# Performance work log

Measured on AMD Instinct MI355X. Metric: run time of the kernel, lower is better.

Reference implementation:

```python
import jax, jax.numpy as jnp
import numpy as np

N_NODES = 100000
N_EDGES = 1_600_000


def setup_inputs() -> dict:
    key = jax.random.key(0)
    ks = jax.random.split(key, 18)
    glorot = lambda k, fi, fo: jax.random.normal(k, (fi, fo), jnp.float32) * np.sqrt(2.0 / (fi + fo))
    inp = {
        "x": jax.random.normal(ks[0], (N_NODES, 5), jnp.float32),
        "edge_index": jax.random.randint(ks[1], (2, N_EDGES), 0, N_NODES, jnp.int64 if jax.config.jax_enable_x64 else jnp.int32),
        "W1": glorot(ks[2], 5, 32),  "b1": jnp.zeros((32,), jnp.float32),
        "W2": glorot(ks[3], 32, 32), "b2": jnp.zeros((32,), jnp.float32),
        "W3": glorot(ks[4], 32, 32), "b3": jnp.zeros((32,), jnp.float32),
        "Wd": glorot(ks[5], 32, 1),  "bd": jnp.zeros((1,), jnp.float32),
        "Wa": glorot(ks[6], 32, 1),  "ba": jnp.zeros((1,), jnp.float32),
        "Wt": glorot(ks[7], 32, 2),  "bt": jnp.zeros((2,), jnp.float32),
        "Wact": glorot(ks[8], 32, 9), "bact": jnp.zeros((9,), jnp.float32),
    }
    return inp


def _gcn_layer(x, row, col, norm, W, b):
    # GCNConv(add_self_loops=False): out[col] += norm * (x @ W)[row], then + bias
    h = x @ W                                  # [N, F_out]
    msg = h[row] * norm[:, None]               # [E, F_out]
    return jax.ops.segment_sum(msg, col, num_segments=N_NODES) + b


def reference(x, edge_index, W1, b1, W2, b2, W3, b3, Wd, bd, Wa, ba, Wt, bt, Wact, bact):
    row, col = edge_index[0], edge_index[1]
    # symmetric gcn normalization: deg over targets (unit edge weights)
    deg = jax.ops.segment_sum(jnp.ones((row.shape[0],), x.dtype), col, num_segments=N_NODES)
    dis = jnp.where(deg > 0, jax.lax.rsqrt(jnp.maximum(deg, 1.0)), 0.0)
    norm = dis[row] * dis[col]                 # [E]

    h = jax.nn.relu(_gcn_layer(x, row, col, norm, W1, b1))   # dropout = identity (eval)
    h = jax.nn.relu(_gcn_layer(h, row, col, norm, W2, b2))
    h = jax.nn.relu(_gcn_layer(h, row, col, norm, W3, b3))

    distance_scores = (h @ Wd + bd)[:, 0]      # [N]
    attention_scores = (h @ Wa + ba)[:, 0]     # [N]
    target_idx = jnp.argmax(attention_scores)
    h_t = h[target_idx]                        # [32]
    target_location_score = h_t @ Wt + bt      # [2]
    action_logits = h_t @ Wact + bact          # [9]
    return distance_scores, attention_scores, target_location_score, action_logits
```

## Files before the change

### kernel.cpp

```cpp
#include <hip/hip_runtime.h>
#include <hip/hip_fp16.h>
#include <math.h>


#define N_NODES 100000
#define F 32
#define BUCKET 64
#define NB ((N_NODES + BUCKET - 1) / BUCKET)
#define NBLK 256
#define SMAX 1536
#define TBKT 32
#define NGRP 8
#define RPG (NBLK / NGRP)

__global__ void hist_kernel(const int* __restrict__ col, int* __restrict__ counts, int E,
                            int* __restrict__ ticket) {
    __shared__ int hist[NB];
    int tid = threadIdx.x, blk = blockIdx.x;
    if (blk == 0 && tid == 0) *ticket = 0;
    for (int i = tid; i < NB; i += 1024) hist[i] = 0;
    __syncthreads();
    int chunk = (((E + NBLK - 1) / NBLK) + 1) & ~1;
    int beg = blk * chunk;
    int end = beg + chunk; if (end > E) end = E;
    int cnt = end - beg; if (cnt < 0) cnt = 0;
    int pairs = cnt >> 1;
    const int2* c2 = (const int2*)(col + beg);
    for (int p = tid; p < pairs; p += 1024) {
        int2 v = c2[p];
        atomicAdd(&hist[v.x >> 6], 1);
        atomicAdd(&hist[v.y >> 6], 1);
    }
    if ((cnt & 1) && tid == 0) atomicAdd(&hist[col[end - 1] >> 6], 1);
    __syncthreads();
    for (int i = tid; i < NB; i += 1024) counts[(size_t)blk * NB + i] = hist[i];
}

__global__ void scan_kernel(int* __restrict__ counts, int* __restrict__ tot,
                            int* __restrict__ bucket_base, int* __restrict__ rowstart,
                            int* __restrict__ ticket) {
    __shared__ int tile[NBLK][TBKT];
    __shared__ int wtot[NGRP][TBKT];
    int tid = threadIdx.x;
    int g = tid >> 5, bl = tid & 31;
    int b = blockIdx.x * TBKT + bl;
    bool valid = (b < NB);
    int jbase = g * RPG;
    int run = 0;
#pragma unroll
    for (int r = 0; r < RPG; r++) {
        int j = jbase + r;
        int v = valid ? counts[(size_t)j * NB + b] : 0;
        tile[j][bl] = run;
        run += v;
    }
    wtot[g][bl] = run;
    __syncthreads();
    int off = 0;
#pragma unroll
    for (int gg = 0; gg < NGRP; gg++) {
        int w = wtot[gg][bl];
        if (gg < g) off += w;
    }
    if (valid) {
#pragma unroll
        for (int r = 0; r < RPG; r++) {
            int j = jbase + r;
            counts[(size_t)j * NB + b] = tile[j][bl] + off;
        }
        if (g == NGRP - 1) tot[b] = off + run;
    }
    __shared__ int lastflag;
    __threadfence();
    __syncthreads();
    if (tid == 0) lastflag = (atomicAdd(ticket, 1) == (int)gridDim.x - 1);
    __syncthreads();
    if (!lastflag) return;
    __threadfence();
    constexpr int PER = (NB + 255) / 256;
    __shared__ int bsum[256];
    int base = tid * PER;
    int loc[PER];
    int s = 0;
#pragma unroll
    for (int k = 0; k < PER; k++) {
        int idx = base + k;
        int v = (idx < NB) ? tot[idx] : 0;
        loc[k] = s;
        s += v;
    }
    bsum[tid] = s;
    __syncthreads();
    for (int off2 = 1; off2 < 256; off2 <<= 1) {
        int v = (tid >= off2) ? bsum[tid - off2] : 0;
        __syncthreads();
        bsum[tid] += v;
        __syncthreads();
    }
    int excl = bsum[tid] - s;
#pragma unroll
    for (int k = 0; k < PER; k++) {
        int idx = base + k;
        if (idx < NB) bucket_base[idx] = excl + loc[k];
    }
    if (tid == 255) {
        bucket_base[NB] = bsum[255];
        rowstart[N_NODES] = bsum[255];
    }
}

__global__ void scatter_kernel(const int* __restrict__ row, const int* __restrict__ col,
                               const int* __restrict__ counts, const int* __restrict__ bucket_base,
                               unsigned* __restrict__ storage, int E) {
    __shared__ int cur[NB];
    int tid = threadIdx.x, blk = blockIdx.x;
    for (int i = tid; i < NB; i += 1024)
        cur[i] = counts[(size_t)blk * NB + i] + bucket_base[i];
    __syncthreads();
    int chunk = (((E + NBLK - 1) / NBLK) + 1) & ~1;
    int beg = blk * chunk;
    int end = beg + chunk; if (end > E) end = E;
    int cnt = end - beg; if (cnt < 0) cnt = 0;
    int pairs = cnt >> 1;
    const int2* c2 = (const int2*)(col + beg);
    const int2* r2 = (const int2*)(row + beg);
    for (int p = tid; p < pairs; p += 1024) {
        int2 c = c2[p];
        int2 r = r2[p];
        int pos0 = atomicAdd(&cur[c.x >> 6], 1);
        storage[pos0] = ((unsigned)(c.x & 63) << 17) | (unsigned)r.x;
        int pos1 = atomicAdd(&cur[c.y >> 6], 1);
        storage[pos1] = ((unsigned)(c.y & 63) << 17) | (unsigned)r.y;
    }
    if ((cnt & 1) && tid == 0) {
        int c = col[end - 1], r = row[end - 1];
        int pos = atomicAdd(&cur[c >> 6], 1);
        storage[pos] = ((unsigned)(c & 63) << 17) | (unsigned)r;
    }
}

__global__ void csr_build_kernel(const unsigned* __restrict__ storage, const int* __restrict__ bucket_base,
                                 int* __restrict__ rowstart, int* __restrict__ csr_src,
                                 float* __restrict__ dis, const float* __restrict__ x,
                                 float* __restrict__ xd, int n) {
    __shared__ unsigned sh[SMAX];
    __shared__ int outloc[SMAX];
    __shared__ int hist[BUCKET];
    __shared__ int pre[BUCKET];
    __shared__ int cur[BUCKET];
    __shared__ float dloc[BUCKET];
    int b = blockIdx.x, tid = threadIdx.x;
    if (tid < BUCKET) hist[tid] = 0;
    __syncthreads();
    int base = bucket_base[b];
    int tot = bucket_base[b + 1] - base;
    if (tot > SMAX) tot = SMAX;
    for (int i = tid; i < tot; i += 256) sh[i] = storage[base + i];
    __syncthreads();
    for (int i = tid; i < tot; i += 256) atomicAdd(&hist[sh[i] >> 17], 1);
    __syncthreads();
    if (tid < BUCKET) pre[tid] = hist[tid];
    __syncthreads();
    for (int off = 1; off < BUCKET; off <<= 1) {
        int v = 0;
        if (tid < BUCKET && tid >= off) v = pre[tid - off];
        __syncthreads();
        if (tid < BUCKET && tid >= off) pre[tid] += v;
        __syncthreads();
    }
    if (tid < BUCKET) {
        int excl = pre[tid] - hist[tid];
        cur[tid] = excl;
        int node = b * BUCKET + tid;
        if (node < n) {
            rowstart[node] = base + excl;
            int d = hist[tid];
            float dv = (d > 0) ? rsqrtf((float)d) : 0.0f;
            dis[node] = dv;
            dloc[tid] = dv;
        }
    }
    __syncthreads();
    for (int i = tid; i < BUCKET * 8; i += 256) {
        int nl = i >> 3, f = i & 7;
        int node = b * BUCKET + nl;
        if (node < n) xd[(size_t)node * 8 + f] = (f < 5) ? dloc[nl] * x[(size_t)node * 5 + f] : 0.0f;
    }
    for (int i = tid; i < tot; i += 256) {
        unsigned p = sh[i];
        int pos = atomicAdd(&cur[p >> 17], 1);
        outloc[pos] = (int)(p & 0x1FFFF);
    }
    __syncthreads();
    for (int i = tid; i < tot; i += 256) csr_src[base + i] = outloc[i];
}

__global__ void layer1_fused(const float* __restrict__ xd, const int* __restrict__ rowstart,
                             const int* __restrict__ csr_src, const float* __restrict__ dis,
                             const float* __restrict__ W1, const float* __restrict__ b1,
                             __half* __restrict__ gda, int n) {
    __shared__ float Ws[5 * F];
    __shared__ float s1s[32][8];
    int tid = threadIdx.x;
    if (tid < 5 * F) Ws[tid] = W1[tid];
    int grp = tid >> 3, f = tid & 7;
    int node = blockIdx.x * 32 + grp;
    float sum = 0.0f;
    if (node < n) {
        int start = rowstart[node], end = rowstart[node + 1];
        float a0 = 0, a1 = 0, a2 = 0, a3 = 0, a4 = 0, a5 = 0, a6 = 0, a7 = 0;
        int i = start;
        for (; i + 7 < end; i += 8) {
            int r0 = csr_src[i], r1 = csr_src[i+1], r2 = csr_src[i+2], r3 = csr_src[i+3];
            int r4 = csr_src[i+4], r5 = csr_src[i+5], r6 = csr_src[i+6], r7 = csr_src[i+7];
            a0 += xd[r0*8+f]; a1 += xd[r1*8+f]; a2 += xd[r2*8+f]; a3 += xd[r3*8+f];
            a4 += xd[r4*8+f]; a5 += xd[r5*8+f]; a6 += xd[r6*8+f]; a7 += xd[r7*8+f];
        }
        for (; i < end; i++) a0 += xd[csr_src[i]*8+f];
        sum = ((a0+a1)+(a2+a3)) + ((a4+a5)+(a6+a7));
    }
    s1s[grp][f] = sum;
    __syncthreads();
    if (node < n) {
        float dv = dis[node];
        float sk0 = dv * s1s[grp][0], sk1 = dv * s1s[grp][1], sk2 = dv * s1s[grp][2];
        float sk3 = dv * s1s[grp][3], sk4 = dv * s1s[grp][4];
        int fb = f * 4;
#pragma unroll
        for (int j = 0; j < 4; j++) {
            int ff = fb + j;
            float acc = b1[ff] + sk0 * Ws[0*F+ff] + sk1 * Ws[1*F+ff] + sk2 * Ws[2*F+ff]
                       + sk3 * Ws[3*F+ff] + sk4 * Ws[4*F+ff];
            float h = acc > 0.0f ? acc : 0.0f;
            gda[(size_t)node * F + ff] = __float2half(dv * h);
        }
    }
}

__device__ __forceinline__ void gather8lane(const uint2* __restrict__ gin2,
                                            const int* __restrict__ csr_src,
                                            int start, int end, int l, int E,
                                            float& a0, float& a1, float& a2, float& a3) {
    a0 = a1 = a2 = a3 = 0.0f;
    int i = start;
    if (i + 8 <= end) {
        int safe = i + l; if (safe > E - 1) safe = E - 1;
        int myidx = csr_src[safe];
        while (i + 8 <= end) {
            int nexti = i + 8;
            int nextidx = 0;
            if (nexti + 8 <= end) {
                int s2 = nexti + l; if (s2 > E - 1) s2 = E - 1;
                nextidx = csr_src[s2];
            }
#pragma unroll
            for (int j = 0; j < 8; j++) {
                int r = __shfl(myidx, j, 8);
                uint2 v = gin2[(size_t)r * 8 + l];
                __half2 h0 = *(__half2*)&v.x;
                __half2 h1 = *(__half2*)&v.y;
                float2 f0 = __half22float2(h0);
                float2 f1 = __half22float2(h1);
                a0 += f0.x; a1 += f0.y; a2 += f1.x; a3 += f1.y;
            }
            myidx = nextidx;
            i = nexti;
        }
    }
    for (; i < end; i++) {
        int r = csr_src[i];
        uint2 v = gin2[(size_t)r * 8 + l];
        __half2 h0 = *(__half2*)&v.x;
        __half2 h1 = *(__half2*)&v.y;
        float2 f0 = __half22float2(h0);
        float2 f1 = __half22float2(h1);
        a0 += f0.x; a1 += f0.y; a2 += f1.x; a3 += f1.y;
    }
}

__global__ void layer_mid_fused(const uint2* __restrict__ gin2, const int* __restrict__ rowstart,
                                const int* __restrict__ csr_src, const float* __restrict__ dis,
                                const float* __restrict__ W, const float* __restrict__ bb,
                                uint2* __restrict__ gout2, int n, int E) {
    __shared__ float Ws[F * F];
    __shared__ float hs[32][F + 1];
    int tid = threadIdx.x;
    for (int i = tid; i < F * F; i += 256) Ws[i] = W[i];
    int grp = tid >> 3;
    int l = tid & 7;
    int node = blockIdx.x * 32 + grp;
    int start = rowstart[node], end = rowstart[node + 1];
    float a0, a1, a2, a3;
    gather8lane(gin2, csr_src, start, end, l, E, a0, a1, a2, a3);
    float dv = dis[node];
    int fb = 4 * l;
    hs[grp][fb]     = dv * a0;
    hs[grp][fb + 1] = dv * a1;
    hs[grp][fb + 2] = dv * a2;
    hs[grp][fb + 3] = dv * a3;
    __syncthreads();
    float acc0 = bb[fb], acc1 = bb[fb+1], acc2 = bb[fb+2], acc3 = bb[fb+3];
#pragma unroll
    for (int k = 0; k < F; k++) {
        float hv = hs[grp][k];
        acc0 += hv * Ws[k*F+fb];
        acc1 += hv * Ws[k*F+fb+1];
        acc2 += hv * Ws[k*F+fb+2];
        acc3 += hv * Ws[k*F+fb+3];
    }
    float h0 = acc0 > 0.0f ? acc0 : 0.0f;
    float h1 = acc1 > 0.0f ? acc1 : 0.0f;
    float h2 = acc2 > 0.0f ? acc2 : 0.0f;
    float h3 = acc3 > 0.0f ? acc3 : 0.0f;
    __half2 o0 = __floats2half2_rn(dv * h0, dv * h1);
    __half2 o1 = __floats2half2_rn(dv * h2, dv * h3);
    uint2 pack;
    pack.x = *(unsigned*)&o0;
    pack.y = *(unsigned*)&o1;
    gout2[(size_t)node * 8 + l] = pack;
}

__global__ void layer_last_fused(const uint2* __restrict__ gin2, const int* __restrict__ rowstart,
                                 const int* __restrict__ csr_src, const float* __restrict__ dis,
                                 const float* __restrict__ W3, const float* __restrict__ b3,
                                 const float* __restrict__ Wd, const float* __restrict__ bd,
                                 const float* __restrict__ Wa, const float* __restrict__ ba,
                                 float* __restrict__ out, float* __restrict__ pmax,
                                 int* __restrict__ pidx, int n, int E) {
    __shared__ float Ws[F * F];
    __shared__ float hs[32][F + 1];
    __shared__ float gmax[32];
    __shared__ int gidx[32];
    int tid = threadIdx.x;
    for (int i = tid; i < F * F; i += 256) Ws[i] = W3[i];
    int grp = tid >> 3;
    int l = tid & 7;
    int node = blockIdx.x * 32 + grp;
    int start = rowstart[node], end = rowstart[node + 1];
    float a0, a1, a2, a3;
    gather8lane(gin2, csr_src, start, end, l, E, a0, a1, a2, a3);
    float dv = dis[node];
    int fb = 4 * l;
    hs[grp][fb]     = dv * a0;
    hs[grp][fb + 1] = dv * a1;
    hs[grp][fb + 2] = dv * a2;
    hs[grp][fb + 3] = dv * a3;
    __syncthreads();
    float acc0 = b3[fb], acc1 = b3[fb+1], acc2 = b3[fb+2], acc3 = b3[fb+3];
#pragma unroll
    for (int k = 0; k < F; k++) {
        float hv = hs[grp][k];
        acc0 += hv * Ws[k*F+fb];
        acc1 += hv * Ws[k*F+fb+1];
        acc2 += hv * Ws[k*F+fb+2];
        acc3 += hv * Ws[k*F+fb+3];
    }
    float h0 = acc0 > 0.0f ? acc0 : 0.0f;
    float h1 = acc1 > 0.0f ? acc1 : 0.0f;
    float h2 = acc2 > 0.0f ? acc2 : 0.0f;
    float h3 = acc3 > 0.0f ? acc3 : 0.0f;
    float dterm = h0 * Wd[fb] + h1 * Wd[fb+1] + h2 * Wd[fb+2] + h3 * Wd[fb+3];
    float aterm = h0 * Wa[fb] + h1 * Wa[fb+1] + h2 * Wa[fb+2] + h3 * Wa[fb+3];
#pragma unroll
    for (int off = 4; off > 0; off >>= 1) {
        dterm += __shfl_xor(dterm, off, 8);
        aterm += __shfl_xor(aterm, off, 8);
    }
    if (l == 0) {
        out[node] = dterm + bd[0];
        float asc = aterm + ba[0];
        out[N_NODES + node] = asc;
        gmax[grp] = asc;
        gidx[grp] = node;
    }
    __syncthreads();
    if (tid == 0) {
        float best = gmax[0]; int bi = gidx[0];
        for (int g = 1; g < 32; g++) {
            if (gmax[g] > best || (gmax[g] == best && gidx[g] < bi)) { best = gmax[g]; bi = gidx[g]; }
        }
        pmax[blockIdx.x] = best;
        pidx[blockIdx.x] = bi;
    }
}

__global__ void final_kernel(const float* __restrict__ pmax, const int* __restrict__ pidx, int nblocks,
                             const __half* __restrict__ gin, const int* __restrict__ rowstart,
                             const int* __restrict__ csr_src, const float* __restrict__ dis,
                             const float* __restrict__ W3, const float* __restrict__ b3,
                             const float* __restrict__ Wt, const float* __restrict__ bt,
                             const float* __restrict__ Wact, const float* __restrict__ bact,
                             float* __restrict__ out) {
    __shared__ float smax[256];
    __shared__ int sidx[256];
    __shared__ float part[8][F];
    __shared__ float hrow[F];
    __shared__ float ht[F];
    int tid = threadIdx.x;
    float best = -INFINITY; int bi = 0x7fffffff;
    for (int i = tid; i < nblocks; i += 256) {
        float v = pmax[i]; int ix = pidx[i];
        if (v > best || (v == best && ix < bi)) { best = v; bi = ix; }
    }
    smax[tid] = best; sidx[tid] = bi;
    __syncthreads();
    for (int st = 128; st > 0; st >>= 1) {
        if (tid < st) {
            float v2 = smax[tid + st]; int i2 = sidx[tid + st];
            if (v2 > smax[tid] || (v2 == smax[tid] && i2 < sidx[tid])) { smax[tid] = v2; sidx[tid] = i2; }
        }
        __syncthreads();
    }
    int target = sidx[0];
    int g = tid >> 5, f = tid & 31;
    int start = rowstart[target], end = rowstart[target + 1];
    float acc = 0.0f;
    for (int i = start + g; i < end; i += 8)
        acc += __half2float(gin[(size_t)csr_src[i] * F + f]);
    part[g][f] = acc;
    __syncthreads();
    if (tid < F) {
        float s = 0.0f;
#pragma unroll
        for (int gg = 0; gg < 8; gg++) s += part[gg][tid];
        hrow[tid] = dis[target] * s;
    }
    __syncthreads();
    if (tid < F) {
        float a = b3[tid];
#pragma unroll
        for (int k = 0; k < F; k++) a += hrow[k] * W3[k*F+tid];
        ht[tid] = a > 0.0f ? a : 0.0f;
    }
    __syncthreads();
    if (tid < 2) {
        float a = bt[tid];
#pragma unroll
        for (int k = 0; k < F; k++) a += ht[k] * Wt[k*2+tid];
        out[2 * N_NODES + tid] = a;
    } else if (tid < 11) {
        int j = tid - 2;
        float a = bact[j];
#pragma unroll
        for (int k = 0; k < F; k++) a += ht[k] * Wact[k*9+j];
        out[2 * N_NODES + 2 + j] = a;
    }
}

extern "C" void kernel_launch(void* const* d_in, const int* in_sizes, int n_in,
                              void* d_out, int out_size, void* d_ws, size_t ws_size,
                              hipStream_t stream) {
    const float* x  = (const float*)d_in[0];
    const int*   ei = (const int*)d_in[1];
    const int E = in_sizes[1] / 2;
    const int* row = ei;
    const int* col = ei + E;
    const float* W1 = (const float*)d_in[2];
    const float* b1 = (const float*)d_in[3];
    const float* W2 = (const float*)d_in[4];
    const float* b2 = (const float*)d_in[5];
    const float* W3 = (const float*)d_in[6];
    const float* b3 = (const float*)d_in[7];
    const float* Wd = (const float*)d_in[8];
    const float* bd = (const float*)d_in[9];
    const float* Wa = (const float*)d_in[10];
    const float* ba = (const float*)d_in[11];
    const float* Wt = (const float*)d_in[12];
    const float* bt = (const float*)d_in[13];
    const float* Wact = (const float*)d_in[14];
    const float* bact = (const float*)d_in[15];

    float* out = (float*)d_out;
    float* ws  = (float*)d_ws;

    float*    dis      = ws;
    float*    xd       = ws + N_NODES;
    __half*   gd_a     = (__half*)(ws + (size_t)17 * N_NODES);
    __half*   gd_b     = (__half*)(ws + (size_t)33 * N_NODES);
    unsigned* storage  = (unsigned*)(ws + (size_t)33 * N_NODES);
    int*      bucket_base = (int*)(ws + (size_t)49 * N_NODES);
    int*      counts   = bucket_base + NB + 1;
    int*      rowstart = counts + NBLK * NB;
    int*      csr_src  = rowstart + N_NODES + 1;
    float*    pmax     = (float*)(csr_src + E);
    int*      pidx     = (int*)(pmax + 12500);
    int*      tot      = pidx + 12500;
    int*      ticket   = tot + NB;

    const int B = 256;
    const int nb32 = (N_NODES + 31) / 32;
    const int nscan = (NB + TBKT - 1) / TBKT;

    hist_kernel<<<NBLK, 1024, 0, stream>>>(col, counts, E, ticket);
    scan_kernel<<<nscan, B, 0, stream>>>(counts, tot, bucket_base, rowstart, ticket);
    scatter_kernel<<<NBLK, 1024, 0, stream>>>(row, col, counts, bucket_base, storage, E);
    csr_build_kernel<<<NB, B, 0, stream>>>(storage, bucket_base, rowstart, csr_src, dis, x, xd, N_NODES);

    layer1_fused<<<nb32, B, 0, stream>>>(xd, rowstart, csr_src, dis, W1, b1, gd_a, N_NODES);

    layer_mid_fused<<<nb32, B, 0, stream>>>((const uint2*)gd_a, rowstart, csr_src, dis,
                                            W2, b2, (uint2*)gd_b, N_NODES, E);

    layer_last_fused<<<nb32, B, 0, stream>>>((const uint2*)gd_b, rowstart, csr_src, dis,
                                             W3, b3, Wd, bd, Wa, ba, out, pmax, pidx, N_NODES, E);
    final_kernel<<<1, B, 0, stream>>>(pmax, pidx, nb32, gd_b, rowstart, csr_src, dis,
                                      W3, b3, Wt, bt, Wact, bact, out);
}
```

Measured before the change: 228.1 us.

## Merge CSR build, three GCN layers and argmax into one cooperative kernel

Replaces the five launches after scatter (CSR build, three layer kernels, final argmax/head) with a single persistent cooperative kernel that loops over tiles and separates phases with grid-wide syncs. Shared memory is a union reused across phases. The aim is to remove per-launch overhead and inter-kernel drain gaps. In exchange, occupancy is capped by the grid size and grid.sync costs are paid, and the old multi-kernel path remains as a fallback if the cooperative launch fails.

```diff
diff --git a/kernel.cpp b/kernel.cpp
--- a/kernel.cpp
+++ b/kernel.cpp
@@ -1,4 +1,5 @@
 #include <hip/hip_runtime.h>
+#include <hip/hip_cooperative_groups.h>
 #include <hip/hip_fp16.h>
 #include <math.h>
 
@@ -12,6 +13,7 @@
 #define TBKT 32
 #define NGRP 8
 #define RPG (NBLK / NGRP)
+#define NT (N_NODES / 32)
 
 __global__ void hist_kernel(const int* __restrict__ col, int* __restrict__ counts, int E,
                             int* __restrict__ ticket) {
@@ -136,6 +138,317 @@
         int c = col[end - 1], r = row[end - 1];
         int pos = atomicAdd(&cur[c >> 6], 1);
         storage[pos] = ((unsigned)(c & 63) << 17) | (unsigned)r;
+    }
+}
+
+__device__ __forceinline__ void gather8lane(const uint2* __restrict__ gin2,
+                                            const int* __restrict__ csr_src,
+                                            int start, int end, int l, int E,
+                                            float& a0, float& a1, float& a2, float& a3) {
+    a0 = a1 = a2 = a3 = 0.0f;
+    int i = start;
+    if (i + 8 <= end) {
+        int safe = i + l; if (safe > E - 1) safe = E - 1;
+        int myidx = csr_src[safe];
+        while (i + 8 <= end) {
+            int nexti = i + 8;
+            int nextidx = 0;
+            if (nexti + 8 <= end) {
+                int s2 = nexti + l; if (s2 > E - 1) s2 = E - 1;
+                nextidx = csr_src[s2];
+            }
+#pragma unroll
+            for (int j = 0; j < 8; j++) {
+                int r = __shfl(myidx, j, 8);
+                uint2 v = gin2[(size_t)r * 8 + l];
+                __half2 h0 = *(__half2*)&v.x;
+                __half2 h1 = *(__half2*)&v.y;
+                float2 f0 = __half22float2(h0);
+                float2 f1 = __half22float2(h1);
+                a0 += f0.x; a1 += f0.y; a2 += f1.x; a3 += f1.y;
+            }
+            myidx = nextidx;
+            i = nexti;
+        }
+    }
+    for (; i < end; i++) {
+        int r = csr_src[i];
+        uint2 v = gin2[(size_t)r * 8 + l];
+        __half2 h0 = *(__half2*)&v.x;
+        __half2 h1 = *(__half2*)&v.y;
+        float2 f0 = __half22float2(h0);
+        float2 f1 = __half22float2(h1);
+        a0 += f0.x; a1 += f0.y; a2 += f1.x; a3 += f1.y;
+    }
+}
+
+struct CoopArgs {
+    const unsigned* storage;
+    const int* bucket_base;
+    int* rowstart;
+    int* csr_src;
+    float* dis;
+    const float* x;
+    float* xd;
+    const float* W1; const float* b1;
+    const float* W2; const float* b2;
+    const float* W3; const float* b3;
+    const float* Wd; const float* bd;
+    const float* Wa; const float* ba;
+    const float* Wt; const float* bt;
+    const float* Wact; const float* bact;
+    __half* gda;
+    __half* gdb;
+    float* out;
+    float* pmax;
+    int* pidx;
+    int E;
+};
+
+union SMem {
+    struct { unsigned sh[SMAX]; int outloc[SMAX]; int hist[BUCKET]; int pre[BUCKET];
+             int cur[BUCKET]; float dloc[BUCKET]; } csr;
+    struct { float Ws[5 * F]; float s1s[32][8]; } l1;
+    struct { float Ws[F * F]; float hs[32][F + 1]; float gmax[32]; int gidx[32]; } lm;
+    struct { float smax[256]; int sidx[256]; float part[8][F]; float hrow[F]; float ht[F]; } fin;
+};
+
+__global__ __launch_bounds__(256, 4) void coop_kernel(CoopArgs a) {
+    cooperative_groups::grid_group gg = cooperative_groups::this_grid();
+    __shared__ SMem sm;
+    int tid = threadIdx.x;
+
+    for (int b = blockIdx.x; b < NB; b += gridDim.x) {
+        if (tid < BUCKET) sm.csr.hist[tid] = 0;
+        __syncthreads();
+        int base = a.bucket_base[b];
+        int tot = a.bucket_base[b + 1] - base;
+        if (tot > SMAX) tot = SMAX;
+        for (int i = tid; i < tot; i += 256) sm.csr.sh[i] = a.storage[base + i];
+        __syncthreads();
+        for (int i = tid; i < tot; i += 256) atomicAdd(&sm.csr.hist[sm.csr.sh[i] >> 17], 1);
+        __syncthreads();
+        if (tid < BUCKET) sm.csr.pre[tid] = sm.csr.hist[tid];
+        __syncthreads();
+        for (int off = 1; off < BUCKET; off <<= 1) {
+            int v = 0;
+            if (tid < BUCKET && tid >= off) v = sm.csr.pre[tid - off];
+            __syncthreads();
+            if (tid < BUCKET && tid >= off) sm.csr.pre[tid] += v;
+            __syncthreads();
+        }
+        if (tid < BUCKET) {
+            int excl = sm.csr.pre[tid] - sm.csr.hist[tid];
+            sm.csr.cur[tid] = excl;
+            int node = b * BUCKET + tid;
+            if (node < N_NODES) {
+                a.rowstart[node] = base + excl;
+                int d = sm.csr.hist[tid];
+                float dv = (d > 0) ? rsqrtf((float)d) : 0.0f;
+                a.dis[node] = dv;
+                sm.csr.dloc[tid] = dv;
+            }
+        }
+        __syncthreads();
+        for (int i = tid; i < BUCKET * 8; i += 256) {
+            int nl = i >> 3, f = i & 7;
+            int node = b * BUCKET + nl;
+            if (node < N_NODES)
+                a.xd[(size_t)node * 8 + f] = (f < 5) ? sm.csr.dloc[nl] * a.x[(size_t)node * 5 + f] : 0.0f;
+        }
+        for (int i = tid; i < tot; i += 256) {
+            unsigned p = sm.csr.sh[i];
+            int pos = atomicAdd(&sm.csr.cur[p >> 17], 1);
+            sm.csr.outloc[pos] = (int)(p & 0x1FFFF);
+        }
+        __syncthreads();
+        for (int i = tid; i < tot; i += 256) a.csr_src[base + i] = sm.csr.outloc[i];
+        __syncthreads();
+    }
+    __threadfence();
+    gg.sync();
+
+    int grp = tid >> 3, l = tid & 7, fb = 4 * l;
+
+    for (int i = tid; i < 5 * F; i += 256) sm.l1.Ws[i] = a.W1[i];
+    for (int t = blockIdx.x; t < NT; t += gridDim.x) {
+        int node = t * 32 + grp;
+        int start = a.rowstart[node], end = a.rowstart[node + 1];
+        float s0 = 0, s1 = 0, s2 = 0, s3 = 0, s4 = 0, s5 = 0, s6 = 0, s7 = 0;
+        int i = start;
+        for (; i + 7 < end; i += 8) {
+            int r0 = a.csr_src[i],   r1 = a.csr_src[i+1], r2 = a.csr_src[i+2], r3 = a.csr_src[i+3];
+            int r4 = a.csr_src[i+4], r5 = a.csr_src[i+5], r6 = a.csr_src[i+6], r7 = a.csr_src[i+7];
+            s0 += a.xd[r0*8+l]; s1 += a.xd[r1*8+l]; s2 += a.xd[r2*8+l]; s3 += a.xd[r3*8+l];
+            s4 += a.xd[r4*8+l]; s5 += a.xd[r5*8+l]; s6 += a.xd[r6*8+l]; s7 += a.xd[r7*8+l];
+        }
+        for (; i < end; i++) s0 += a.xd[a.csr_src[i]*8+l];
+        sm.l1.s1s[grp][l] = ((s0+s1)+(s2+s3)) + ((s4+s5)+(s6+s7));
+        __syncthreads();
+        float dv = a.dis[node];
+        float sk0 = dv * sm.l1.s1s[grp][0], sk1 = dv * sm.l1.s1s[grp][1], sk2 = dv * sm.l1.s1s[grp][2];
+        float sk3 = dv * sm.l1.s1s[grp][3], sk4 = dv * sm.l1.s1s[grp][4];
+#pragma unroll
+        for (int j = 0; j < 4; j++) {
+            int ff = fb + j;
+            float acc = a.b1[ff] + sk0 * sm.l1.Ws[0*F+ff] + sk1 * sm.l1.Ws[1*F+ff]
+                       + sk2 * sm.l1.Ws[2*F+ff] + sk3 * sm.l1.Ws[3*F+ff] + sk4 * sm.l1.Ws[4*F+ff];
+            float h = acc > 0.0f ? acc : 0.0f;
+            a.gda[(size_t)node * F + ff] = __float2half(dv * h);
+        }
+        __syncthreads();
+    }
+    __threadfence();
+    gg.sync();
+
+    {
+        const uint2* gin2 = (const uint2*)a.gda;
+        for (int i = tid; i < F * F; i += 256) sm.lm.Ws[i] = a.W2[i];
+        for (int t = blockIdx.x; t < NT; t += gridDim.x) {
+            int node = t * 32 + grp;
+            int start = a.rowstart[node], end = a.rowstart[node + 1];
+            float a0, a1, a2, a3;
+            gather8lane(gin2, a.csr_src, start, end, l, a.E, a0, a1, a2, a3);
+            float dv = a.dis[node];
+            sm.lm.hs[grp][fb]     = dv * a0;
+            sm.lm.hs[grp][fb + 1] = dv * a1;
+            sm.lm.hs[grp][fb + 2] = dv * a2;
+            sm.lm.hs[grp][fb + 3] = dv * a3;
+            __syncthreads();
+            float acc0 = a.b2[fb], acc1 = a.b2[fb+1], acc2 = a.b2[fb+2], acc3 = a.b2[fb+3];
+#pragma unroll
+            for (int k = 0; k < F; k++) {
+                float hv = sm.lm.hs[grp][k];
+                acc0 += hv * sm.lm.Ws[k*F+fb];
+                acc1 += hv * sm.lm.Ws[k*F+fb+1];
+                acc2 += hv * sm.lm.Ws[k*F+fb+2];
+                acc3 += hv * sm.lm.Ws[k*F+fb+3];
+            }
+            float h0 = acc0 > 0.0f ? acc0 : 0.0f;
+            float h1 = acc1 > 0.0f ? acc1 : 0.0f;
+            float h2 = acc2 > 0.0f ? acc2 : 0.0f;
+            float h3 = acc3 > 0.0f ? acc3 : 0.0f;
+            __half2 o0 = __floats2half2_rn(dv * h0, dv * h1);
+            __half2 o1 = __floats2half2_rn(dv * h2, dv * h3);
+            uint2 pack;
+            pack.x = *(unsigned*)&o0;
+            pack.y = *(unsigned*)&o1;
+            ((uint2*)a.gdb)[(size_t)node * 8 + l] = pack;
+            __syncthreads();
+        }
+    }
+    __threadfence();
+    gg.sync();
+
+    {
+        const uint2* gin2 = (const uint2*)a.gdb;
+        for (int i = tid; i < F * F; i += 256) sm.lm.Ws[i] = a.W3[i];
+        for (int t = blockIdx.x; t < NT; t += gridDim.x) {
+            int node = t * 32 + grp;
+            int start = a.rowstart[node], end = a.rowstart[node + 1];
+            float a0, a1, a2, a3;
+            gather8lane(gin2, a.csr_src, start, end, l, a.E, a0, a1, a2, a3);
+            float dv = a.dis[node];
+            sm.lm.hs[grp][fb]     = dv * a0;
+            sm.lm.hs[grp][fb + 1] = dv * a1;
+            sm.lm.hs[grp][fb + 2] = dv * a2;
+            sm.lm.hs[grp][fb + 3] = dv * a3;
+            __syncthreads();
+            float acc0 = a.b3[fb], acc1 = a.b3[fb+1], acc2 = a.b3[fb+2], acc3 = a.b3[fb+3];
+#pragma unroll
+            for (int k = 0; k < F; k++) {
+                float hv = sm.lm.hs[grp][k];
+                acc0 += hv * sm.lm.Ws[k*F+fb];
+                acc1 += hv * sm.lm.Ws[k*F+fb+1];
+                acc2 += hv * sm.lm.Ws[k*F+fb+2];
+                acc3 += hv * sm.lm.Ws[k*F+fb+3];
+            }
+            float h0 = acc0 > 0.0f ? acc0 : 0.0f;
+            float h1 = acc1 > 0.0f ? acc1 : 0.0f;
+            float h2 = acc2 > 0.0f ? acc2 : 0.0f;
+            float h3 = acc3 > 0.0f ? acc3 : 0.0f;
+            float dterm = h0 * a.Wd[fb] + h1 * a.Wd[fb+1] + h2 * a.Wd[fb+2] + h3 * a.Wd[fb+3];
+            float aterm = h0 * a.Wa[fb] + h1 * a.Wa[fb+1] + h2 * a.Wa[fb+2] + h3 * a.Wa[fb+3];
+#pragma unroll
+            for (int off = 4; off > 0; off >>= 1) {
+                dterm += __shfl_xor(dterm, off, 8);
+                aterm += __shfl_xor(aterm, off, 8);
+            }
+            if (l == 0) {
+                a.out[node] = dterm + a.bd[0];
+                float asc = aterm + a.ba[0];
+                a.out[N_NODES + node] = asc;
+                sm.lm.gmax[grp] = asc;
+                sm.lm.gidx[grp] = node;
+            }
+            __syncthreads();
+            if (tid == 0) {
+                float best = sm.lm.gmax[0]; int bi = sm.lm.gidx[0];
+                for (int g2 = 1; g2 < 32; g2++) {
+                    if (sm.lm.gmax[g2] > best || (sm.lm.gmax[g2] == best && sm.lm.gidx[g2] < bi)) {
+                        best = sm.lm.gmax[g2]; bi = sm.lm.gidx[g2];
+                    }
+                }
+                a.pmax[t] = best;
+                a.pidx[t] = bi;
+            }
+            __syncthreads();
+        }
+    }
+    __threadfence();
+    gg.sync();
+
+    if (blockIdx.x == 0) {
+        float best = -INFINITY; int bi = 0x7fffffff;
+        for (int i = tid; i < NT; i += 256) {
+            float v = a.pmax[i]; int ix = a.pidx[i];
+            if (v > best || (v == best && ix < bi)) { best = v; bi = ix; }
+        }
+        sm.fin.smax[tid] = best; sm.fin.sidx[tid] = bi;
+        __syncthreads();
+        for (int st = 128; st > 0; st >>= 1) {
+            if (tid < st) {
+                float v2 = sm.fin.smax[tid + st]; int i2 = sm.fin.sidx[tid + st];
+                if (v2 > sm.fin.smax[tid] || (v2 == sm.fin.smax[tid] && i2 < sm.fin.sidx[tid])) {
+                    sm.fin.smax[tid] = v2; sm.fin.sidx[tid] = i2;
+                }
+            }
+            __syncthreads();
+        }
+        int target = sm.fin.sidx[0];
+        int g = tid >> 5, f = tid & 31;
+        int start = a.rowstart[target], end = a.rowstart[target + 1];
+        float acc = 0.0f;
+        for (int i = start + g; i < end; i += 8)
+            acc += __half2float(a.gdb[(size_t)a.csr_src[i] * F + f]);
+        sm.fin.part[g][f] = acc;
+        __syncthreads();
+        if (tid < F) {
+            float s = 0.0f;
+#pragma unroll
+            for (int g2 = 0; g2 < 8; g2++) s += sm.fin.part[g2][tid];
+            sm.fin.hrow[tid] = a.dis[target] * s;
+        }
+        __syncthreads();
+        if (tid < F) {
+            float v = a.b3[tid];
+#pragma unroll
+            for (int k = 0; k < F; k++) v += sm.fin.hrow[k] * a.W3[k*F+tid];
+            sm.fin.ht[tid] = v > 0.0f ? v : 0.0f;
+        }
+        __syncthreads();
+        if (tid < 2) {
+            float v = a.bt[tid];
+#pragma unroll
+            for (int k = 0; k < F; k++) v += sm.fin.ht[k] * a.Wt[k*2+tid];
+            a.out[2 * N_NODES + tid] = v;
+        } else if (tid < 11) {
+            int j = tid - 2;
+            float v = a.bact[j];
+#pragma unroll
+            for (int k = 0; k < F; k++) v += sm.fin.ht[k] * a.Wact[k*9+j];
+            a.out[2 * N_NODES + 2 + j] = v;
+        }
     }
 }
 
@@ -234,47 +547,6 @@
             float h = acc > 0.0f ? acc : 0.0f;
             gda[(size_t)node * F + ff] = __float2half(dv * h);
         }
-    }
-}
-
-__device__ __forceinline__ void gather8lane(const uint2* __restrict__ gin2,
-                                            const int* __restrict__ csr_src,
-                                            int start, int end, int l, int E,
-                                            float& a0, float& a1, float& a2, float& a3) {
-    a0 = a1 = a2 = a3 = 0.0f;
-    int i = start;
-    if (i + 8 <= end) {
-        int safe = i + l; if (safe > E - 1) safe = E - 1;
-        int myidx = csr_src[safe];
-        while (i + 8 <= end) {
-            int nexti = i + 8;
-            int nextidx = 0;
-            if (nexti + 8 <= end) {
-                int s2 = nexti + l; if (s2 > E - 1) s2 = E - 1;
-                nextidx = csr_src[s2];
-            }
-#pragma unroll
-            for (int j = 0; j < 8; j++) {
-                int r = __shfl(myidx, j, 8);
-                uint2 v = gin2[(size_t)r * 8 + l];
-                __half2 h0 = *(__half2*)&v.x;
-                __half2 h1 = *(__half2*)&v.y;
-                float2 f0 = __half22float2(h0);
-                float2 f1 = __half22float2(h1);
-                a0 += f0.x; a1 += f0.y; a2 += f1.x; a3 += f1.y;
-            }
-            myidx = nextidx;
-            i = nexti;
-        }
-    }
-    for (; i < end; i++) {
-        int r = csr_src[i];
-        uint2 v = gin2[(size_t)r * 8 + l];
-        __half2 h0 = *(__half2*)&v.x;
-        __half2 h1 = *(__half2*)&v.y;
-        float2 f0 = __half22float2(h0);
-        float2 f1 = __half22float2(h1);
-        a0 += f0.x; a1 += f0.y; a2 += f1.x; a3 += f1.y;
     }
 }
 
@@ -494,15 +766,41 @@
     hist_kernel<<<NBLK, 1024, 0, stream>>>(col, counts, E, ticket);
     scan_kernel<<<nscan, B, 0, stream>>>(counts, tot, bucket_base, rowstart, ticket);
     scatter_kernel<<<NBLK, 1024, 0, stream>>>(row, col, counts, bucket_base, storage, E);
-    csr_build_kernel<<<NB, B, 0, stream>>>(storage, bucket_base, rowstart, csr_src, dis, x, xd, N_NODES);
-
-    layer1_fused<<<nb32, B, 0, stream>>>(xd, rowstart, csr_src, dis, W1, b1, gd_a, N_NODES);
-
-    layer_mid_fused<<<nb32, B, 0, stream>>>((const uint2*)gd_a, rowstart, csr_src, dis,
-                                            W2, b2, (uint2*)gd_b, N_NODES, E);
-
-    layer_last_fused<<<nb32, B, 0, stream>>>((const uint2*)gd_b, rowstart, csr_src, dis,
-                                             W3, b3, Wd, bd, Wa, ba, out, pmax, pidx, N_NODES, E);
-    final_kernel<<<1, B, 0, stream>>>(pmax, pidx, nb32, gd_b, rowstart, csr_src, dis,
-                                      W3, b3, Wt, bt, Wact, bact, out);
-}
+
+    static int coop_blocks = -1;
+    if (coop_blocks < 0) {
+        int bpc = 0;
+        if (hipOccupancyMaxActiveBlocksPerMultiprocessor(&bpc, coop_kernel, 256, 0) != hipSuccess || bpc <= 0)
+            bpc = 2;
+        int nCU = 256;
+        hipDeviceProp_t prop;
+        if (hipGetDeviceProperties(&prop, 0) == hipSuccess && prop.multiProcessorCount > 0)
+            nCU = prop.multiProcessorCount;
+        long g = (long)bpc * nCU;
+        if (g > 2048) g = 2048;
+        if (g < 64) g = 64;
+        coop_blocks = (int)g;
+    }
+
+    CoopArgs ca;
+    ca.storage = storage; ca.bucket_base = bucket_base; ca.rowstart = rowstart;
+    ca.csr_src = csr_src; ca.dis = dis; ca.x = x; ca.xd = xd;
+    ca.W1 = W1; ca.b1 = b1; ca.W2 = W2; ca.b2 = b2; ca.W3 = W3; ca.b3 = b3;
+    ca.Wd = Wd; ca.bd = bd; ca.Wa = Wa; ca.ba = ba; ca.Wt = Wt; ca.bt = bt;
+    ca.Wact = Wact; ca.bact = bact;
+    ca.gda = gd_a; ca.gdb = gd_b; ca.out = out; ca.pmax = pmax; ca.pidx = pidx; ca.E = E;
+    void* kargs[] = { &ca };
+
+    hipError_t cerr = hipLaunchCooperativeKernel(coop_kernel, dim3(coop_blocks), dim3(256),
+                                                 kargs, 0, stream);
+    if (cerr != hipSuccess) {
+        csr_build_kernel<<<NB, B, 0, stream>>>(storage, bucket_base, rowstart, csr_src, dis, x, xd, N_NODES);
+        layer1_fused<<<nb32, B, 0, stream>>>(xd, rowstart, csr_src, dis, W1, b1, gd_a, N_NODES);
+        layer_mid_fused<<<nb32, B, 0, stream>>>((const uint2*)gd_a, rowstart, csr_src, dis,
+                                                W2, b2, (uint2*)gd_b, N_NODES, E);
+        layer_last_fused<<<nb32, B, 0, stream>>>((const uint2*)gd_b, rowstart, csr_src, dis,
+                                                 W3, b3, Wd, bd, Wa, ba, out, pmax, pidx, N_NODES, E);
+        final_kernel<<<1, B, 0, stream>>>(pmax, pidx, nb32, gd_b, rowstart, csr_src, dis,
+                                          W3, b3, Wt, bt, Wact, bact, out);
+    }
+}
```

Result: slower. 757.5 us (+232.1%).

## Software-pipeline neighbor gathers and fuse final reduction into last layer

Applied to the files above, without the earlier changes.

The 8-lane gather now issues all eight feature loads for the next chunk of neighbors before accumulating the current chunk. This double-buffers in registers to keep more memory requests in flight. Separately, the final argmax and head kernel is folded into layer_last_fused with a last-block-done atomic ticket, which removes one kernel launch. The cost is higher register pressure and a serial tail on the final block.

```diff
diff --git a/kernel.cpp b/kernel.cpp
--- a/kernel.cpp
+++ b/kernel.cpp
@@ -14,10 +14,10 @@
 #define RPG (NBLK / NGRP)
 
 __global__ void hist_kernel(const int* __restrict__ col, int* __restrict__ counts, int E,
-                            int* __restrict__ ticket) {
+                            int* __restrict__ ticket, int* __restrict__ ticket2) {
     __shared__ int hist[NB];
     int tid = threadIdx.x, blk = blockIdx.x;
-    if (blk == 0 && tid == 0) *ticket = 0;
+    if (blk == 0 && tid == 0) { *ticket = 0; *ticket2 = 0; }
     for (int i = tid; i < NB; i += 1024) hist[i] = 0;
     __syncthreads();
     int chunk = (((E + NBLK - 1) / NBLK) + 1) & ~1;
@@ -237,43 +237,51 @@
     }
 }
 
-__device__ __forceinline__ void gather8lane(const uint2* __restrict__ gin2,
+__device__ __forceinline__ void gather8pipe(const uint2* __restrict__ gin2,
                                             const int* __restrict__ csr_src,
                                             int start, int end, int l, int E,
                                             float& a0, float& a1, float& a2, float& a3) {
     a0 = a1 = a2 = a3 = 0.0f;
-    int i = start;
-    if (i + 8 <= end) {
-        int safe = i + l; if (safe > E - 1) safe = E - 1;
-        int myidx = csr_src[safe];
-        while (i + 8 <= end) {
-            int nexti = i + 8;
-            int nextidx = 0;
-            if (nexti + 8 <= end) {
-                int s2 = nexti + l; if (s2 > E - 1) s2 = E - 1;
-                nextidx = csr_src[s2];
+    int nfull = (end - start) >> 3;
+    if (nfull > 0) {
+        uint2 v[8];
+        int s0 = start + l; if (s0 > E - 1) s0 = E - 1;
+        int idx = csr_src[s0];
+#pragma unroll
+        for (int j = 0; j < 8; j++) {
+            int r = __shfl(idx, j, 8);
+            v[j] = gin2[(size_t)r * 8 + l];
+        }
+        for (int k = 1; k < nfull; k++) {
+            int sk = start + 8 * k + l;
+            int idxn = csr_src[sk];
+            uint2 w[8];
+#pragma unroll
+            for (int j = 0; j < 8; j++) {
+                int r = __shfl(idxn, j, 8);
+                w[j] = gin2[(size_t)r * 8 + l];
             }
 #pragma unroll
             for (int j = 0; j < 8; j++) {
-                int r = __shfl(myidx, j, 8);
-                uint2 v = gin2[(size_t)r * 8 + l];
-                __half2 h0 = *(__half2*)&v.x;
-                __half2 h1 = *(__half2*)&v.y;
-                float2 f0 = __half22float2(h0);
-                float2 f1 = __half22float2(h1);
+                float2 f0 = __half22float2(*(__half2*)&v[j].x);
+                float2 f1 = __half22float2(*(__half2*)&v[j].y);
                 a0 += f0.x; a1 += f0.y; a2 += f1.x; a3 += f1.y;
             }
-            myidx = nextidx;
-            i = nexti;
-        }
-    }
-    for (; i < end; i++) {
+#pragma unroll
+            for (int j = 0; j < 8; j++) v[j] = w[j];
+        }
+#pragma unroll
+        for (int j = 0; j < 8; j++) {
+            float2 f0 = __half22float2(*(__half2*)&v[j].x);
+            float2 f1 = __half22float2(*(__half2*)&v[j].y);
+            a0 += f0.x; a1 += f0.y; a2 += f1.x; a3 += f1.y;
+        }
+    }
+    for (int i = start + 8 * nfull; i < end; i++) {
         int r = csr_src[i];
-        uint2 v = gin2[(size_t)r * 8 + l];
-        __half2 h0 = *(__half2*)&v.x;
-        __half2 h1 = *(__half2*)&v.y;
-        float2 f0 = __half22float2(h0);
-        float2 f1 = __half22float2(h1);
+        uint2 vv = gin2[(size_t)r * 8 + l];
+        float2 f0 = __half22float2(*(__half2*)&vv.x);
+        float2 f1 = __half22float2(*(__half2*)&vv.y);
         a0 += f0.x; a1 += f0.y; a2 += f1.x; a3 += f1.y;
     }
 }
@@ -291,7 +299,7 @@
     int node = blockIdx.x * 32 + grp;
     int start = rowstart[node], end = rowstart[node + 1];
     float a0, a1, a2, a3;
-    gather8lane(gin2, csr_src, start, end, l, E, a0, a1, a2, a3);
+    gather8pipe(gin2, csr_src, start, end, l, E, a0, a1, a2, a3);
     float dv = dis[node];
     int fb = 4 * l;
     hs[grp][fb]     = dv * a0;
@@ -325,8 +333,11 @@
                                  const float* __restrict__ W3, const float* __restrict__ b3,
                                  const float* __restrict__ Wd, const float* __restrict__ bd,
                                  const float* __restrict__ Wa, const float* __restrict__ ba,
+                                 const float* __restrict__ Wt, const float* __restrict__ bt,
+                                 const float* __restrict__ Wact, const float* __restrict__ bact,
                                  float* __restrict__ out, float* __restrict__ pmax,
-                                 int* __restrict__ pidx, int n, int E) {
+                                 int* __restrict__ pidx, int* __restrict__ ticket2,
+                                 int n, int E) {
     __shared__ float Ws[F * F];
     __shared__ float hs[32][F + 1];
     __shared__ float gmax[32];
@@ -338,7 +349,7 @@
     int node = blockIdx.x * 32 + grp;
     int start = rowstart[node], end = rowstart[node + 1];
     float a0, a1, a2, a3;
-    gather8lane(gin2, csr_src, start, end, l, E, a0, a1, a2, a3);
+    gather8pipe(gin2, csr_src, start, end, l, E, a0, a1, a2, a3);
     float dv = dis[node];
     int fb = 4 * l;
     hs[grp][fb]     = dv * a0;
@@ -382,21 +393,19 @@
         pmax[blockIdx.x] = best;
         pidx[blockIdx.x] = bi;
     }
-}
-
-__global__ void final_kernel(const float* __restrict__ pmax, const int* __restrict__ pidx, int nblocks,
-                             const __half* __restrict__ gin, const int* __restrict__ rowstart,
-                             const int* __restrict__ csr_src, const float* __restrict__ dis,
-                             const float* __restrict__ W3, const float* __restrict__ b3,
-                             const float* __restrict__ Wt, const float* __restrict__ bt,
-                             const float* __restrict__ Wact, const float* __restrict__ bact,
-                             float* __restrict__ out) {
+    __shared__ int lastflag;
+    __threadfence();
+    __syncthreads();
+    if (tid == 0) lastflag = (atomicAdd(ticket2, 1) == (int)gridDim.x - 1);
+    __syncthreads();
+    if (!lastflag) return;
+    __threadfence();
     __shared__ float smax[256];
     __shared__ int sidx[256];
     __shared__ float part[8][F];
     __shared__ float hrow[F];
     __shared__ float ht[F];
-    int tid = threadIdx.x;
+    int nblocks = gridDim.x;
     float best = -INFINITY; int bi = 0x7fffffff;
     for (int i = tid; i < nblocks; i += 256) {
         float v = pmax[i]; int ix = pidx[i];
@@ -413,9 +422,10 @@
     }
     int target = sidx[0];
     int g = tid >> 5, f = tid & 31;
-    int start = rowstart[target], end = rowstart[target + 1];
+    const __half* gin = (const __half*)gin2;
+    int tstart = rowstart[target], tend = rowstart[target + 1];
     float acc = 0.0f;
-    for (int i = start + g; i < end; i += 8)
+    for (int i = tstart + g; i < tend; i += 8)
         acc += __half2float(gin[(size_t)csr_src[i] * F + f]);
     part[g][f] = acc;
     __syncthreads();
@@ -486,12 +496,13 @@
     int*      pidx     = (int*)(pmax + 12500);
     int*      tot      = pidx + 12500;
     int*      ticket   = tot + NB;
+    int*      ticket2  = ticket + 1;
 
     const int B = 256;
     const int nb32 = (N_NODES + 31) / 32;
     const int nscan = (NB + TBKT - 1) / TBKT;
 
-    hist_kernel<<<NBLK, 1024, 0, stream>>>(col, counts, E, ticket);
+    hist_kernel<<<NBLK, 1024, 0, stream>>>(col, counts, E, ticket, ticket2);
     scan_kernel<<<nscan, B, 0, stream>>>(counts, tot, bucket_base, rowstart, ticket);
     scatter_kernel<<<NBLK, 1024, 0, stream>>>(row, col, counts, bucket_base, storage, E);
     csr_build_kernel<<<NB, B, 0, stream>>>(storage, bucket_base, rowstart, csr_src, dis, x, xd, N_NODES);
@@ -502,7 +513,6 @@
                                             W2, b2, (uint2*)gd_b, N_NODES, E);
 
     layer_last_fused<<<nb32, B, 0, stream>>>((const uint2*)gd_b, rowstart, csr_src, dis,
-                                             W3, b3, Wd, bd, Wa, ba, out, pmax, pidx, N_NODES, E);
-    final_kernel<<<1, B, 0, stream>>>(pmax, pidx, nb32, gd_b, rowstart, csr_src, dis,
-                                      W3, b3, Wt, bt, Wact, bact, out);
-}
+                                             W3, b3, Wd, bd, Wa, ba, Wt, bt, Wact, bact,
+                                             out, pmax, pidx, ticket2, N_NODES, E);
+}
```

Result: slower. 424.0 us (+85.9%).
